# Performance work log

Measured on AMD Instinct MI355X. Metric: run time of the kernel, lower is better.

## Reference

```python
import jax, jax.numpy as jnp
import numpy as np

INNER_DIM = 512
SCALE = 1.0 / np.sqrt(INNER_DIM).astype(np.float32)  # module scales by 1/sqrt(inner_dim), not head_dim


def setup_inputs() -> dict:
    key = jax.random.key(0)
    ks = jax.random.split(key, 7)
    b, n, d = 4, 4096, 512
    s = 0.02
    return {
        "x": jax.random.normal(ks[0], (b, n, d), jnp.float32),
        "y": jax.random.normal(ks[1], (b, n, d), jnp.float32),
        "Wq": jax.random.normal(ks[2], (INNER_DIM, d), jnp.float32) * s,  # torch Linear weight [out, in]
        "Wk": jax.random.normal(ks[3], (INNER_DIM, d), jnp.float32) * s,
        "Wv": jax.random.normal(ks[4], (INNER_DIM, d), jnp.float32) * s,
        "Wo": jax.random.normal(ks[5], (d, INNER_DIM), jnp.float32) * s,
        "bo": jax.random.normal(ks[6], (d,), jnp.float32) * s,
    }


def reference(x, y, Wq, Wk, Wv, Wo, bo):
    # q, k from x; v from y (bias-free projections)
    q = jnp.einsum('bnd,id->bni', x, Wq)
    k = jnp.einsum('bnd,id->bni', x, Wk)
    v = jnp.einsum('bnd,id->bni', y, Wv)
    # full [b, n, n] scores, scaled by 1/sqrt(inner_dim)
    alpha = jnp.einsum('bik,bjk->bij', q, k) * SCALE
    alpha = jax.nn.softmax(alpha, axis=-1)
    ctx = jnp.einsum('bij,bjd->bid', alpha, v)
    out = jnp.einsum('bid,od->bio', ctx, Wo) + bo
    return out
```

## Files before the change

kernel.cpp:

```cpp
#include <hip/hip_runtime.h>
#include <hip/hip_bf16.h>


typedef unsigned short u16;
typedef __bf16 bf16x8 __attribute__((ext_vector_type(8)));
typedef float f32x4 __attribute__((ext_vector_type(4)));

#define SCALE_QK 0.044194173824159216f

__device__ __forceinline__ u16 f2bf(float f) {
    __hip_bfloat16 h = __float2bfloat16(f);
    return __builtin_bit_cast(u16, h);
}

__device__ __forceinline__ void load_lds16(const void* g, void* l) {
    __builtin_amdgcn_global_load_lds(
        (const __attribute__((address_space(1))) void*)g,
        (__attribute__((address_space(3))) void*)l, 16, 0, 0);
}

__global__ void cvt_bf16_kernel(const float* __restrict__ src, u16* __restrict__ dst,
                                int n8, float scale) {
    int i = blockIdx.x * blockDim.x + threadIdx.x;
    if (i >= n8) return;
    const float4* s4 = (const float4*)src;
    float4 v0 = s4[2 * i], v1 = s4[2 * i + 1];
    union { u16 u[8]; uint4 v; } o;
    o.u[0] = f2bf(v0.x * scale); o.u[1] = f2bf(v0.y * scale);
    o.u[2] = f2bf(v0.z * scale); o.u[3] = f2bf(v0.w * scale);
    o.u[4] = f2bf(v1.x * scale); o.u[5] = f2bf(v1.y * scale);
    o.u[6] = f2bf(v1.z * scale); o.u[7] = f2bf(v1.w * scale);
    ((uint4*)dst)[i] = o.v;
}

__global__ void wvo_kernel(const float* __restrict__ Wo, const float* __restrict__ Wv,
                           float* __restrict__ Wvo) {
    int o = blockIdx.x, t = threadIdx.x;
    float a0 = 0.f, a1 = 0.f;
    for (int i = 0; i < 512; ++i) {
        float w = Wo[o * 512 + i];
        a0 += w * Wv[i * 512 + t];
        a1 += w * Wv[i * 512 + t + 256];
    }
    Wvo[o * 512 + t] = a0;
    Wvo[o * 512 + t + 256] = a1;
}

template <int EPI>
__launch_bounds__(256)
__global__ void gemm_bt_kernel(const u16* __restrict__ A, const u16* __restrict__ B,
                               void* __restrict__ Cout, int N, int K, int lda, int ldb,
                               long long sAz, long long sBz, long long sCz) {
    __shared__ u16 As[2][128 * 32];
    __shared__ u16 Bs[2][128 * 32];

    const int tid = threadIdx.x;
    const int wave = tid >> 6, lane = tid & 63;
    const int lr = lane & 15, lg = lane >> 4;
    const int wr = wave >> 1, wc = wave & 1;

    const int gx = gridDim.x, gy = gridDim.y;
    int bid = (blockIdx.z * gy + blockIdx.y) * gx + blockIdx.x;
    const int nwg = gx * gy * gridDim.z;
    int lgc = (bid & 7) * (nwg >> 3) + (bid >> 3);
    const int bx = lgc % gx;
    int rem = lgc / gx;
    const int by = rem % gy, z = rem / gy;
    const int row0 = by * 128, col0 = bx * 128;

    const u16* Ab = A + (size_t)z * sAz;
    const u16* Bb = B + (size_t)z * sBz;

    f32x4 acc[4][4];
#pragma unroll
    for (int i = 0; i < 4; ++i)
#pragma unroll
        for (int j = 0; j < 4; ++j) acc[i][j] = (f32x4){0.f, 0.f, 0.f, 0.f};

    const int KT = K >> 5;

#define STAGE(bufi, kt2)                                                          \
    {                                                                             \
        _Pragma("unroll") for (int i = 0; i < 2; ++i) {                           \
            int chunk = i * 256 + tid;                                            \
            int r = chunk >> 2, c4 = chunk & 3;                                   \
            load_lds16(Ab + (size_t)(row0 + r) * lda + (kt2) * 32 + c4 * 8,       \
                       &As[bufi][(i * 256 + wave * 64) * 8]);                     \
            load_lds16(Bb + (size_t)(col0 + r) * ldb + (kt2) * 32 + c4 * 8,       \
                       &Bs[bufi][(i * 256 + wave * 64) * 8]);                     \
        }                                                                         \
    }

    STAGE(0, 0);
    int buf = 0;
    for (int kt = 0; kt < KT; ++kt) {
        __syncthreads();
        if (kt + 1 < KT) STAGE(buf ^ 1, kt + 1);

        bf16x8 af[4], bfr[4];
#pragma unroll
        for (int mf = 0; mf < 4; ++mf)
            af[mf] = *(const bf16x8*)&As[buf][(wr * 64 + mf * 16 + lr) * 32 + lg * 8];
#pragma unroll
        for (int nf = 0; nf < 4; ++nf)
            bfr[nf] = *(const bf16x8*)&Bs[buf][(wc * 64 + nf * 16 + lr) * 32 + lg * 8];
#pragma unroll
        for (int mf = 0; mf < 4; ++mf)
#pragma unroll
            for (int nf = 0; nf < 4; ++nf)
                acc[mf][nf] = __builtin_amdgcn_mfma_f32_16x16x32_bf16(
                    af[mf], bfr[nf], acc[mf][nf], 0, 0, 0);
        buf ^= 1;
    }
#undef STAGE

    const int rbase = row0 + wr * 64;
    const int cbase = col0 + wc * 64;

    if (EPI == 0 || EPI == 2) {
        u16* C = (u16*)Cout + (size_t)z * sCz;
#pragma unroll
        for (int mf = 0; mf < 4; ++mf)
#pragma unroll
            for (int nf = 0; nf < 4; ++nf)
#pragma unroll
                for (int reg = 0; reg < 4; ++reg) {
                    int r = rbase + mf * 16 + lg * 4 + reg;
                    int c = cbase + nf * 16 + lr;
                    float v = acc[mf][nf][reg];
                    if (EPI == 2) v = __expf(v);
                    C[(size_t)r * N + c] = f2bf(v);
                }
    } else {
        u16* C = (u16*)Cout;
#pragma unroll
        for (int mf = 0; mf < 4; ++mf)
#pragma unroll
            for (int nf = 0; nf < 4; ++nf) {
                int rg = rbase + mf * 16 + lg * 4;
                int bsel = rg >> 12, rl = rg & 4095;
                int c = cbase + nf * 16 + lr;
                union { u16 u[4]; uint2 v; } o;
#pragma unroll
                for (int reg = 0; reg < 4; ++reg) o.u[reg] = f2bf(acc[mf][nf][reg]);
                *(uint2*)(C + ((size_t)bsel << 21) + ((size_t)c << 12) + rl) = o.v;
            }
    }
}

__launch_bounds__(512, 4)
__global__ void pv_kernel(const u16* __restrict__ P, const u16* __restrict__ vwT,
                          float* __restrict__ part, float* __restrict__ lpart) {
    __shared__ u16 As[2][64 * 32];
    __shared__ u16 Bs[2][512 * 32];

    const int tid = threadIdx.x;
    const int wave = tid >> 6, lane = tid & 63;
    const int lr = lane & 15, lg = lane >> 4;

    int bid = blockIdx.x;
    int lgc = (bid & 7) * 64 + (bid >> 3);
    const int rp = lgc & 63;
    const int ks = (lgc >> 6) & 1;
    const int z = lgc >> 7;
    const int row0 = rp * 64;

    const u16* Pz = P + (size_t)z * 16777216 + (size_t)row0 * 4096 + ks * 2048;
    const u16* Vz = vwT + (size_t)z * 2097152 + ks * 2048;

    f32x4 acc[4][4];
#pragma unroll
    for (int i = 0; i < 4; ++i)
#pragma unroll
        for (int j = 0; j < 4; ++j) acc[i][j] = (f32x4){0.f, 0.f, 0.f, 0.f};
    float rs = 0.f;

#define STAGE(bufi, kt2)                                                          \
    {                                                                             \
        if (tid < 256) {                                                          \
            int r = tid >> 2, c4 = tid & 3;                                       \
            load_lds16(Pz + (size_t)r * 4096 + (kt2) * 32 + c4 * 8,               \
                       &As[bufi][wave * 512]);                                    \
        }                                                                         \
        _Pragma("unroll") for (int it = 0; it < 4; ++it) {                        \
            int c = it * 512 + tid;                                               \
            int r = c >> 2, c4 = c & 3;                                           \
            load_lds16(Vz + (size_t)r * 4096 + (kt2) * 32 + c4 * 8,               \
                       &Bs[bufi][(it * 512 + wave * 64) * 8]);                    \
        }                                                                         \
    }

    STAGE(0, 0);
    int buf = 0;
    for (int kt = 0; kt < 64; ++kt) {
        __syncthreads();
        if (kt + 1 < 64) STAGE(buf ^ 1, kt + 1);

        {
            uint2 rv = *(const uint2*)&As[buf][(tid >> 3) * 32 + (tid & 7) * 4];
            rs += __uint_as_float(rv.x << 16) + __uint_as_float(rv.x & 0xffff0000u) +
                  __uint_as_float(rv.y << 16) + __uint_as_float(rv.y & 0xffff0000u);
        }

        bf16x8 af[4];
#pragma unroll
        for (int mf = 0; mf < 4; ++mf)
            af[mf] = *(const bf16x8*)&As[buf][(mf * 16 + lr) * 32 + lg * 8];
#pragma unroll
        for (int nf = 0; nf < 4; ++nf) {
            bf16x8 bfr = *(const bf16x8*)&Bs[buf][(wave * 64 + nf * 16 + lr) * 32 + lg * 8];
#pragma unroll
            for (int mf = 0; mf < 4; ++mf)
                acc[mf][nf] = __builtin_amdgcn_mfma_f32_16x16x32_bf16(
                    af[mf], bfr, acc[mf][nf], 0, 0, 0);
        }
        buf ^= 1;
    }
#undef STAGE

    rs += __shfl_xor(rs, 1, 64);
    rs += __shfl_xor(rs, 2, 64);
    rs += __shfl_xor(rs, 4, 64);
    if ((tid & 7) == 0)
        lpart[(size_t)ks * 16384 + z * 4096 + row0 + (tid >> 3)] = rs;

    float* O = part + (size_t)ks * 8388608 + ((size_t)z * 4096 + row0) * 512;
#pragma unroll
    for (int mf = 0; mf < 4; ++mf)
#pragma unroll
        for (int nf = 0; nf < 4; ++nf) {
            int c = wave * 64 + nf * 16 + lr;
#pragma unroll
            for (int reg = 0; reg < 4; ++reg) {
                int r = mf * 16 + lg * 4 + reg;
                O[(size_t)r * 512 + c] = acc[mf][nf][reg];
            }
        }
}

__global__ void reduce_kernel(const float* __restrict__ part,
                              const float* __restrict__ lpart,
                              const float* __restrict__ bo,
                              float* __restrict__ out) {
    int i = blockIdx.x * blockDim.x + threadIdx.x;
    int r = i >> 7, c4 = i & 127;
    float inv = 1.0f / (lpart[r] + lpart[16384 + r]);
    float4 a = ((const float4*)part)[i];
    float4 b = ((const float4*)part)[i + 2097152];
    float4 bi = ((const float4*)bo)[c4];
    float4 o;
    o.x = (a.x + b.x) * inv + bi.x;
    o.y = (a.y + b.y) * inv + bi.y;
    o.z = (a.z + b.z) * inv + bi.z;
    o.w = (a.w + b.w) * inv + bi.w;
    ((float4*)out)[i] = o;
}

extern "C" void kernel_launch(void* const* d_in, const int* in_sizes, int n_in,
                              void* d_out, int out_size, void* d_ws, size_t ws_size,
                              hipStream_t stream) {
    const float* x  = (const float*)d_in[0];
    const float* y  = (const float*)d_in[1];
    const float* Wq = (const float*)d_in[2];
    const float* Wk = (const float*)d_in[3];
    const float* Wv = (const float*)d_in[4];
    const float* Wo = (const float*)d_in[5];
    const float* bo = (const float*)d_in[6];
    float* out = (float*)d_out;

    char* ws = (char*)d_ws;
    u16*   xb   = (u16*)(ws + 0);
    u16*   yb   = (u16*)(ws + 16777216);
    u16*   qk   = (u16*)(ws + 33554432);
    float* part = (float*)(ws + 0);
    u16*   vwT  = (u16*)(ws + 67108864);
    u16*   Wqkb = (u16*)(ws + 83886080);
    u16*   Wvob = (u16*)(ws + 84934656);
    float* Wvo  = (float*)(ws + 85458944);
    float* lpart= (float*)(ws + 86507520);
    u16*   P    = (u16*)(ws + 86638592);

    cvt_bf16_kernel<<<4096, 256, 0, stream>>>(x, xb, 1048576, 1.0f);
    cvt_bf16_kernel<<<4096, 256, 0, stream>>>(y, yb, 1048576, 1.0f);
    cvt_bf16_kernel<<<128, 256, 0, stream>>>(Wq, Wqkb, 32768, SCALE_QK);
    cvt_bf16_kernel<<<128, 256, 0, stream>>>(Wk, Wqkb + 262144, 32768, 1.0f);

    wvo_kernel<<<512, 256, 0, stream>>>(Wo, Wv, Wvo);
    cvt_bf16_kernel<<<128, 256, 0, stream>>>(Wvo, Wvob, 32768, 1.0f);

    gemm_bt_kernel<0><<<dim3(8, 128, 1), 256, 0, stream>>>(xb, Wqkb, qk,
                                                           1024, 512, 512, 512, 0, 0, 0);
    gemm_bt_kernel<1><<<dim3(4, 128, 1), 256, 0, stream>>>(yb, Wvob, vwT,
                                                           512, 512, 512, 512, 0, 0, 0);

    gemm_bt_kernel<2><<<dim3(32, 32, 4), 256, 0, stream>>>(qk, qk + 512, P,
                                                           4096, 512, 1024, 1024,
                                                           4194304, 4194304, 16777216);

    pv_kernel<<<512, 512, 0, stream>>>(P, vwT, part, lpart);

    reduce_kernel<<<8192, 256, 0, stream>>>(part, lpart, bo, out);
}
```

Baseline: 318.1 us.

## Replace QK^T exp GEMM with 256x256-tile, 8-wave deeply pipelined kernel

Adds a dedicated score GEMM using 256x256 output tiles with 8 waves, an 8-slot LDS ring of half-k-step stages loaded via global_load_lds with XOR swizzle, explicit vmcnt waits, barriers and setprio around MFMA blocks. The exp epilogue moves into this kernel and the generic kernel drops EPI==2. Larger tiles raise arithmetic intensity and the multi-stage prefetch aims to hide global latency. The cost is higher register and LDS pressure (128 KB LDS, launch bounds of 2 blocks per CU) and fragile hand-tuned wait counts.

```diff
diff --git a/kernel.cpp b/kernel.cpp
--- a/kernel.cpp
+++ b/kernel.cpp
@@ -46,6 +46,129 @@
     Wvo[o * 512 + t + 256] = a1;
 }
 
+__launch_bounds__(512, 2)
+__global__ void gemm256_exp_kernel(const u16* __restrict__ A, const u16* __restrict__ B,
+                                   u16* __restrict__ Cout, int N, int lda, int ldb,
+                                   long long sAz, long long sBz, long long sCz) {
+    __shared__ u16 lds[8][8192];
+
+    const int tid = threadIdx.x;
+    const int wave = tid >> 6, lane = tid & 63;
+    const int lr = lane & 15, lg = lane >> 4;
+    const int wm = wave >> 2, wn = wave & 3;
+
+    int bid = (blockIdx.z * gridDim.y + blockIdx.y) * gridDim.x + blockIdx.x;
+    int lgc = (bid & 7) * 128 + (bid >> 3);
+    const int bx = lgc & 15;
+    int rem = lgc >> 4;
+    const int by = rem & 15, z = rem >> 4;
+    const int row0 = by * 256, col0 = bx * 256;
+
+    const u16* Ab = A + (size_t)z * sAz;
+    const u16* Bb = B + (size_t)z * sBz;
+
+    const int rb = lane >> 2;
+    const int kg8 = ((lane & 3) ^ (rb & 3)) << 3;
+
+    f32x4 acc[8][4];
+#pragma unroll
+    for (int i = 0; i < 8; ++i)
+#pragma unroll
+        for (int j = 0; j < 4; ++j) acc[i][j] = (f32x4){0.f, 0.f, 0.f, 0.f};
+
+#define STAGE_HALF(s_, slot_)                                                     \
+    {                                                                             \
+        const int h_ = (s_)&3, ts_ = (s_) >> 2;                                   \
+        const u16* G_ = (h_ & 1) ? Bb : Ab;                                       \
+        const int pan_ = (h_ & 1) ? col0 : row0;                                  \
+        const int ld_ = (h_ & 1) ? ldb : lda;                                     \
+        const int kofs_ = ts_ * 64 + (h_ >> 1) * 32 + kg8;                        \
+        _Pragma("unroll") for (int j_ = 0; j_ < 2; ++j_) {                        \
+            int r_ = (j_ * 8 + wave) * 16 + rb;                                   \
+            load_lds16(G_ + (size_t)(pan_ + r_) * ld_ + kofs_,                    \
+                       &lds[slot_][(j_ * 8 + wave) * 512]);                       \
+        }                                                                         \
+    }
+
+    #pragma unroll
+    for (int s = 0; s < 6; ++s) STAGE_HALF(s, s);
+    asm volatile("s_waitcnt vmcnt(4)");
+    __builtin_amdgcn_sched_barrier(0);
+    __builtin_amdgcn_s_barrier();
+
+    bf16x8 bfr[4];
+
+#pragma unroll
+    for (int i = 0; i < 4; ++i) {
+#pragma unroll
+        for (int p = 0; p < 8; ++p) {
+            const int q = p & 3;
+            const int ks = q >> 1;
+            const int aslot = (p >> 2) * 4 + 2 * ks;
+            const int bslot = aslot + 1;
+            const int fmb = (q & 1) * 4;
+
+            bf16x8 af[4];
+#pragma unroll
+            for (int f = 0; f < 4; ++f) {
+                int row = wm * 128 + (fmb + f) * 16 + lr;
+                af[f] = *(const bf16x8*)&lds[aslot][row * 32 + ((lg ^ (lr & 3)) << 3)];
+            }
+            if (q == 0 || q == 2) {
+#pragma unroll
+                for (int f = 0; f < 4; ++f) {
+                    int row = wn * 64 + f * 16 + lr;
+                    bfr[f] = *(const bf16x8*)&lds[bslot][row * 32 + ((lg ^ (lr & 3)) << 3)];
+                }
+            }
+
+            {
+                const int s = 8 * i + p + 6;
+                if (s < 32) {
+                    const int slot = (p + 6) & 7;
+                    STAGE_HALF(s, slot);
+                }
+            }
+
+            __builtin_amdgcn_sched_barrier(0);
+            __builtin_amdgcn_s_barrier();
+            asm volatile("s_waitcnt lgkmcnt(0)");
+            __builtin_amdgcn_sched_barrier(0);
+
+            __builtin_amdgcn_s_setprio(1);
+#pragma unroll
+            for (int f = 0; f < 4; ++f)
+#pragma unroll
+                for (int n = 0; n < 4; ++n)
+                    acc[fmb + f][n] = __builtin_amdgcn_mfma_f32_16x16x32_bf16(
+                        af[f], bfr[n], acc[fmb + f][n], 0, 0, 0);
+            __builtin_amdgcn_s_setprio(0);
+
+            if (p == 3) {
+                if (i == 3) asm volatile("s_waitcnt vmcnt(0)");
+                else        asm volatile("s_waitcnt vmcnt(4)");
+            } else if (p == 7 && i < 3) {
+                asm volatile("s_waitcnt vmcnt(4)");
+            }
+            __builtin_amdgcn_sched_barrier(0);
+            __builtin_amdgcn_s_barrier();
+        }
+    }
+#undef STAGE_HALF
+
+    u16* C = Cout + (size_t)z * sCz;
+#pragma unroll
+    for (int fm = 0; fm < 8; ++fm)
+#pragma unroll
+        for (int fn = 0; fn < 4; ++fn)
+#pragma unroll
+            for (int reg = 0; reg < 4; ++reg) {
+                int r = row0 + wm * 128 + fm * 16 + lg * 4 + reg;
+                int c = col0 + wn * 64 + fn * 16 + lr;
+                C[(size_t)r * N + c] = f2bf(__expf(acc[fm][fn][reg]));
+            }
+}
+
 template <int EPI>
 __launch_bounds__(256)
 __global__ void gemm_bt_kernel(const u16* __restrict__ A, const u16* __restrict__ B,
@@ -117,7 +240,7 @@
     const int rbase = row0 + wr * 64;
     const int cbase = col0 + wc * 64;
 
-    if (EPI == 0 || EPI == 2) {
+    if (EPI == 0) {
         u16* C = (u16*)Cout + (size_t)z * sCz;
 #pragma unroll
         for (int mf = 0; mf < 4; ++mf)
@@ -127,9 +250,7 @@
                 for (int reg = 0; reg < 4; ++reg) {
                     int r = rbase + mf * 16 + lg * 4 + reg;
                     int c = cbase + nf * 16 + lr;
-                    float v = acc[mf][nf][reg];
-                    if (EPI == 2) v = __expf(v);
-                    C[(size_t)r * N + c] = f2bf(v);
+                    C[(size_t)r * N + c] = f2bf(acc[mf][nf][reg]);
                 }
     } else {
         u16* C = (u16*)Cout;
@@ -293,9 +414,9 @@
     gemm_bt_kernel<1><<<dim3(4, 128, 1), 256, 0, stream>>>(yb, Wvob, vwT,
                                                            512, 512, 512, 512, 0, 0, 0);
 
-    gemm_bt_kernel<2><<<dim3(32, 32, 4), 256, 0, stream>>>(qk, qk + 512, P,
-                                                           4096, 512, 1024, 1024,
-                                                           4194304, 4194304, 16777216);
+    gemm256_exp_kernel<<<dim3(16, 16, 4), 512, 0, stream>>>(qk, qk + 512, P,
+                                                            4096, 1024, 1024,
+                                                            4194304, 4194304, 16777216);
 
     pv_kernel<<<512, 512, 0, stream>>>(P, vwT, part, lpart);
 
```

Result: no change. 315.8 us (-0.7%).
